# Optimization experiments

Measured on AMD Instinct MI355X. Metric: run time of the kernel, lower is better.

## Reference

```python
import jax, jax.numpy as jnp
import numpy as np

NDIM = (256, 256, 256)
NMIN = (-1.0, -1.0, -1.0)
NMAX = (1.0, 1.0, 1.0)
NDELTA = tuple((NMAX[i] - NMIN[i]) / (NDIM[i] - 1.0) for i in range(3))
MIN_DEG, MAX_DEG = 0, 10
ANNEALED_ALPHA = 1.0
EPS = 1e-12


def compute_grad(grid):
    # central differences on the voxel grid with edge padding -> [N, 3]
    g = grid.reshape(NDIM[0], NDIM[1], NDIM[2])
    p = jnp.pad(g, ((1, 1), (1, 1), (1, 1)), mode='edge')
    dx = (p[2:, 1:-1, 1:-1] - p[:-2, 1:-1, 1:-1]) / (2.0 * NDELTA[0])
    dy = (p[1:-1, 2:, 1:-1] - p[1:-1, :-2, 1:-1]) / (2.0 * NDELTA[1])
    dz = (p[1:-1, 1:-1, 2:] - p[1:-1, 1:-1, :-2]) / (2.0 * NDELTA[2])
    return jnp.stack([dx, dy, dz], axis=-1).reshape(-1, 3)


def trilinear3(data, pts):
    # data: [N, 4] flattened voxel features, pts: [B, 3] -> [B, 4]
    x = (pts[..., 0] - NMIN[0]) / NDELTA[0]
    y = (pts[..., 1] - NMIN[1]) / NDELTA[1]
    z = (pts[..., 2] - NMIN[2]) / NDELTA[2]
    x0f = jnp.floor(x); y0f = jnp.floor(y); z0f = jnp.floor(z)
    xd = (x - x0f)[..., None]
    yd = (y - y0f)[..., None]
    zd = (z - z0f)[..., None]
    x0 = jnp.clip(x0f.astype(jnp.int32), 0, NDIM[0] - 1)
    x1 = jnp.clip(x0f.astype(jnp.int32) + 1, 0, NDIM[0] - 1)
    y0 = jnp.clip(y0f.astype(jnp.int32), 0, NDIM[1] - 1)
    y1 = jnp.clip(y0f.astype(jnp.int32) + 1, 0, NDIM[1] - 1)
    z0 = jnp.clip(z0f.astype(jnp.int32), 0, NDIM[2] - 1)
    z1 = jnp.clip(z0f.astype(jnp.int32) + 1, 0, NDIM[2] - 1)
    sYZ, sZ = NDIM[1] * NDIM[2], NDIM[2]
    gat = lambda i, j, k: data[sYZ * i + sZ * j + k]
    c00 = gat(x0, y0, z0) * (1 - xd) + gat(x1, y0, z0) * xd
    c01 = gat(x0, y0, z1) * (1 - xd) + gat(x1, y0, z1) * xd
    c10 = gat(x0, y1, z0) * (1 - xd) + gat(x1, y1, z0) * xd
    c11 = gat(x0, y1, z1) * (1 - xd) + gat(x1, y1, z1) * xd
    c0 = c00 * (1 - yd) + c10 * yd
    c1 = c01 * (1 - yd) + c11 * yd
    return c0 * (1 - zd) + c1 * zd


def annealed_pos_enc(x, alpha):
    # nerfies-style windowed positional encoding with identity concat
    bands = jnp.arange(MIN_DEG, MAX_DEG, dtype=x.dtype)  # [D]
    scales = 2.0 ** bands
    xb = x[..., None, :] * scales[:, None]               # [..., D, 3]
    four = jnp.sin(jnp.stack([xb, xb + 0.5 * jnp.pi], axis=-2))  # [..., D, 2, 3]
    w = jnp.clip(alpha - bands, 0.0, 1.0)
    w = 0.5 * (1.0 - jnp.cos(jnp.pi * w))                # cosine easing window
    four = four * w[:, None, None]
    four = four.reshape(x.shape[:-1] + (-1,))            # [..., D*6]
    return jnp.concatenate([x, four], axis=-1)           # [..., 3 + D*6]


def mlp(feats, w0, b0, w1, b1, w2, b2, w3, b3, wo, bo):
    # net_depth=4, skip_layer=2 -> concat inputs after layer index 2
    h = jax.nn.relu(feats @ w0 + b0)
    h = jax.nn.relu(h @ w1 + b1)
    h = jax.nn.relu(h @ w2 + b2)
    h = jnp.concatenate([h, feats], axis=-1)
    h = jax.nn.relu(h @ w3 + b3)
    return h @ wo + bo


def safe_l2_norm(v):
    return jnp.sqrt(jnp.sum(v * v, axis=-1, keepdims=True) + EPS)


def setup_inputs() -> dict:
    key = jax.random.key(0)
    ks = jax.random.split(key, 8)
    B = 1048576
    N = NDIM[0] * NDIM[1] * NDIM[2]
    x = jax.random.uniform(ks[0], (B, 3), jnp.float32, -1.0, 1.0)
    grid = jax.random.normal(ks[1], (N, 1), jnp.float32)
    glorot = lambda k, fi, fo: jax.random.normal(k, (fi, fo), jnp.float32) * jnp.sqrt(2.0 / (fi + fo))
    return {
        'x': x, 'grid': grid,
        'w0': glorot(ks[2], 63, 128), 'b0': jnp.zeros((128,), jnp.float32),
        'w1': glorot(ks[3], 128, 128), 'b1': jnp.zeros((128,), jnp.float32),
        'w2': glorot(ks[4], 128, 128), 'b2': jnp.zeros((128,), jnp.float32),
        'w3': glorot(ks[5], 191, 128), 'b3': jnp.zeros((128,), jnp.float32),
        'wo': jax.random.normal(ks[6], (128, 3), jnp.float32) * 1e-5,  # output_init normal(1e-5)
        'bo': jnp.zeros((3,), jnp.float32),
    }


def reference(x, grid, w0, b0, w1, b1, w2, b2, w3, b3, wo, bo):
    data = jnp.concatenate([grid, compute_grad(grid)], axis=-1)  # [N, 4]
    ret = trilinear3(data, x)                                    # [B, 4]
    feats = annealed_pos_enc(x[:, None], ANNEALED_ALPHA * MAX_DEG)  # [B, 1, 63]
    raw = mlp(feats, w0, b0, w1, b1, w2, b2, w3, b3, wo, bo)[:, 0]  # [B, 3]
    # residual + direct output: rotate gradient vector by axis-angle raw
    theta = safe_l2_norm(raw)
    e = raw / theta
    cond = ret[..., 1:]
    a = safe_l2_norm(cond)
    v = cond / a
    rot = a * (jnp.cos(theta) * v + jnp.sin(theta) * jnp.cross(e, v)
               + (1.0 - jnp.cos(theta)) * jnp.sum(e * v, axis=-1, keepdims=True) * e)
    return (ret[..., :1], ret[..., 1:], rot)
```

## Files before the change

### kernel.cpp

```cpp
#include <hip/hip_runtime.h>


typedef __attribute__((ext_vector_type(4))) float f4;
typedef long long llg;

__device__ __forceinline__ float bf2f(unsigned int u) {
    union { float f; unsigned int i; } v; v.i = u << 16; return v.f;
}
__device__ __forceinline__ unsigned short f2bf(float f) {
    union { float f; unsigned int i; } v; v.f = f;
    unsigned int x = v.i;
    return (unsigned short)((x + 0x7fffu + ((x >> 16) & 1u)) >> 16);
}
__device__ __forceinline__ unsigned int pkbf(float a, float b) {
    unsigned int r;
    asm("v_cvt_pk_bf16_f32 %0, %1, %2" : "=v"(r) : "v"(a), "v"(b));
    return r;
}
__device__ __forceinline__ float gv(const float* __restrict__ g, int i, int j, int k) {
    return g[(i * 256 + j) * 256 + k];
}
__device__ __forceinline__ int featmap(int kp) {
    if (kp < 3) return kp;
    if (kp == 3) return -1;
    const int m = kp - 4, b = m / 6, r = m - 6 * b, d = r >> 1, c = r & 1;
    return 3 + 6 * b + 3 * c + d;
}

#define WS_TOTAL 67584
#define SWZ_BLOCKS 264
#define DG_BLOCKS 8192
#define DG_OFF_SH 131072
#define WS_NEED (262144ull + 16777216ull * 8ull)
#define WO_SCALE 8192.0f
#define WO_INV   (1.0f / 8192.0f)

__global__ __launch_bounds__(256) void prep(
    const float* __restrict__ g,
    const float* __restrict__ w0, const float* __restrict__ w1,
    const float* __restrict__ w2, const float* __restrict__ w3,
    const float* __restrict__ wo,
    unsigned char* __restrict__ ws8, unsigned short* __restrict__ dg,
    int do_dgrid)
{
    const int bid = blockIdx.x;
    if (bid < SWZ_BLOCKS) {
        int idx = bid * 256 + threadIdx.x;
        const float* src; int base, NT, Kact, Nact, ld;
        if (idx < 8192)       { src = w0; base = 0;     NT = 8; Kact = 64;  Nact = 128; ld = 128; }
        else if (idx < 24576) { src = w1; base = 8192;  NT = 8; Kact = 128; Nact = 128; ld = 128; }
        else if (idx < 40960) { src = w2; base = 24576; NT = 8; Kact = 128; Nact = 128; ld = 128; }
        else if (idx < 65536) { src = w3; base = 40960; NT = 8; Kact = 192; Nact = 128; ld = 128; }
        else                  { src = wo; base = 65536; NT = 1; Kact = 128; Nact = 3;   ld = 3;   }
        int local = idx - base;
        int j = local & 7;
        int lane = (local >> 3) & 63;
        int chunk = local >> 9;
        int nt = chunk % NT, kt = chunk / NT;
        int k = kt * 32 + ((lane >> 4) << 3) + j;
        int n = nt * 16 + (lane & 15);
        float v = 0.0f;
        if (k < Kact && n < Nact) {
            int ko = k;
            if (base == 0)            ko = featmap(k);
            else if (base == 40960 && k >= 128) {
                int f = featmap(k - 128);
                ko = (f < 0) ? -1 : 128 + f;
            }
            if (ko >= 0) v = src[ko * ld + n];
            if (base == 65536) v *= WO_SCALE;
        }
        int p = __builtin_amdgcn_cvt_pk_fp8_f32(v, v, 0, false);
        ws8[idx] = (unsigned char)(p & 0xff);
    } else if (do_dgrid) {
        const int t  = (bid - SWZ_BLOCKS) * 256 + threadIdx.x;
        const int k0 = (t & 31) << 3;
        const int j  = (t >> 5) & 255;
        const int i  = t >> 13;
        const float* row = g + (i * 256 + j) * 256;
        const float* rxp = g + (min(i + 1, 255) * 256 + j) * 256;
        const float* rxm = g + (max(i - 1, 0)   * 256 + j) * 256;
        const float* ryp = g + (i * 256 + min(j + 1, 255)) * 256;
        const float* rym = g + (i * 256 + max(j - 1, 0))   * 256;
        float se[8], sxp[8], sxm[8], syp[8], sym[8];
        {
            f4 a = *(const f4*)(row + k0), b = *(const f4*)(row + k0 + 4);
            #pragma unroll
            for (int q = 0; q < 4; ++q) { se[q] = a[q]; se[q + 4] = b[q]; }
            a = *(const f4*)(rxp + k0); b = *(const f4*)(rxp + k0 + 4);
            #pragma unroll
            for (int q = 0; q < 4; ++q) { sxp[q] = a[q]; sxp[q + 4] = b[q]; }
            a = *(const f4*)(rxm + k0); b = *(const f4*)(rxm + k0 + 4);
            #pragma unroll
            for (int q = 0; q < 4; ++q) { sxm[q] = a[q]; sxm[q + 4] = b[q]; }
            a = *(const f4*)(ryp + k0); b = *(const f4*)(ryp + k0 + 4);
            #pragma unroll
            for (int q = 0; q < 4; ++q) { syp[q] = a[q]; syp[q + 4] = b[q]; }
            a = *(const f4*)(rym + k0); b = *(const f4*)(rym + k0 + 4);
            #pragma unroll
            for (int q = 0; q < 4; ++q) { sym[q] = a[q]; sym[q + 4] = b[q]; }
        }
        float zv[10];
        zv[0] = row[max(k0 - 1, 0)];
        #pragma unroll
        for (int q = 0; q < 8; ++q) zv[q + 1] = se[q];
        zv[9] = row[min(k0 + 8, 255)];
        unsigned int o[16];
        #pragma unroll
        for (int q = 0; q < 8; ++q) {
            o[q * 2 + 0] = pkbf(se[q], (sxp[q] - sxm[q]) * 63.75f);
            o[q * 2 + 1] = pkbf((syp[q] - sym[q]) * 63.75f, (zv[q + 2] - zv[q]) * 63.75f);
        }
        unsigned short* dst = dg + (size_t)(((i * 256 + j) * 256 + k0)) * 4;
        #pragma unroll
        for (int q = 0; q < 4; ++q)
            *(uint4*)(dst + q * 8) = *(const uint4*)(&o[q * 4]);
    }
}

#define HSTRIDE_B 136
#define FSTRIDE_B 88
#define WV_BYTES (32 * HSTRIDE_B + 32 * FSTRIDE_B)

template<bool FAST>
__global__ __launch_bounds__(256, 5) void voxmlp(
    const float* __restrict__ x, const float* __restrict__ grid,
    const unsigned char* __restrict__ ws8, const unsigned short* __restrict__ dg,
    const float* __restrict__ b0, const float* __restrict__ b1,
    const float* __restrict__ b2, const float* __restrict__ b3,
    const float* __restrict__ bo,
    float* __restrict__ out, int B)
{
    __shared__ unsigned char smem[WV_BYTES * 4];

    const int lane = threadIdx.x & 63;
    const int wave = threadIdx.x >> 6;
    const int quad = lane >> 4;
    const int lm   = lane & 15;
    unsigned char* bufH = smem + wave * WV_BYTES;
    unsigned char* fbuf = bufH + 32 * HSTRIDE_B;

    const int pbase = blockIdx.x * 128 + wave * 32;

    const int p2   = lane & 31;
    const int role = lane >> 5;
    const int pid  = pbase + p2;

    const float px = x[pid * 3 + 0];
    const float py = x[pid * 3 + 1];
    const float pz = x[pid * 3 + 2];

    if (role == 0) {
        const float fx = (px + 1.0f) * 127.5f;
        const float fy = (py + 1.0f) * 127.5f;
        const float fz = (pz + 1.0f) * 127.5f;
        const float fx0 = floorf(fx), fy0 = floorf(fy), fz0 = floorf(fz);
        const float xd = fx - fx0, yd = fy - fy0, zd = fz - fz0;
        const int ix0 = min(max((int)fx0, 0), 255);
        const int iy0 = min(max((int)fy0, 0), 255);
        const int iz0 = min(max((int)fz0, 0), 255);
        const int ix1 = min(ix0 + 1, 255);
        const int iy1 = min(iy0 + 1, 255);
        const int iz1 = min(iz0 + 1, 255);

        float ret0 = 0.f, c1 = 0.f, c2 = 0.f, c3 = 0.f;
        if (FAST) {
            #pragma unroll
            for (int c = 0; c < 8; ++c) {
                const int i = (c & 4) ? ix1 : ix0;
                const int j = (c & 2) ? iy1 : iy0;
                const int k = (c & 1) ? iz1 : iz0;
                const float wgt = ((c & 4) ? xd : 1.0f - xd) *
                                  ((c & 2) ? yd : 1.0f - yd) *
                                  ((c & 1) ? zd : 1.0f - zd);
                const uint2 w = *(const uint2*)(dg + (size_t)((i * 256 + j) * 256 + k) * 4);
                ret0 = fmaf(wgt, bf2f(w.x & 0xffffu), ret0);
                c1   = fmaf(wgt, bf2f(w.x >> 16),     c1);
                c2   = fmaf(wgt, bf2f(w.y & 0xffffu), c2);
                c3   = fmaf(wgt, bf2f(w.y >> 16),     c3);
            }
        } else {
            #pragma unroll
            for (int c = 0; c < 8; ++c) {
                const int i = (c & 4) ? ix1 : ix0;
                const int j = (c & 2) ? iy1 : iy0;
                const int k = (c & 1) ? iz1 : iz0;
                const float wgt = ((c & 4) ? xd : 1.0f - xd) *
                                  ((c & 2) ? yd : 1.0f - yd) *
                                  ((c & 1) ? zd : 1.0f - zd);
                const float v  = gv(grid, i, j, k);
                const float gx = (gv(grid, min(i + 1, 255), j, k) - gv(grid, max(i - 1, 0), j, k)) * 63.75f;
                const float gy = (gv(grid, i, min(j + 1, 255), k) - gv(grid, i, max(j - 1, 0), k)) * 63.75f;
                const float gz = (gv(grid, i, j, min(k + 1, 255)) - gv(grid, i, j, max(k - 1, 0))) * 63.75f;
                ret0 = fmaf(wgt, v,  ret0);
                c1   = fmaf(wgt, gx, c1);
                c2   = fmaf(wgt, gy, c2);
                c3   = fmaf(wgt, gz, c3);
            }
        }
        out[pid] = ret0;
        out[B + pid * 3 + 0] = c1;
        out[B + pid * 3 + 1] = c2;
        out[B + pid * 3 + 2] = c3;
        float* cst = (float*)(fbuf + p2 * FSTRIDE_B + 64);
        cst[0] = c1; cst[1] = c2; cst[2] = c3;
    } else {
        float s[64];
        s[0] = px; s[1] = py; s[2] = pz; s[3] = 0.0f;
        const float crd[3] = {px, py, pz};
        float sc = 1.0f;
        #pragma unroll
        for (int b = 0; b < 10; ++b) {
            #pragma unroll
            for (int d = 0; d < 3; ++d) {
                float sv, cv;
                __sincosf(crd[d] * sc, &sv, &cv);
                s[4 + b * 6 + d * 2 + 0] = sv;
                s[4 + b * 6 + d * 2 + 1] = cv;
            }
            sc *= 2.0f;
        }
        unsigned int dw[16];
        #pragma unroll
        for (int i = 0; i < 16; ++i) {
            int d = __builtin_amdgcn_cvt_pk_fp8_f32(s[4 * i + 0], s[4 * i + 1], 0, false);
            d     = __builtin_amdgcn_cvt_pk_fp8_f32(s[4 * i + 2], s[4 * i + 3], d, true);
            dw[i] = (unsigned int)d;
        }
        unsigned char* fb = fbuf + p2 * FSTRIDE_B;
        #pragma unroll
        for (int i = 0; i < 4; ++i) {
            uint2 pk; pk.x = dw[2 * i]; pk.y = dw[2 * i + 1];
            *(uint2*)(fb + i * 8) = pk;
        }
        #pragma unroll
        for (int i = 4; i < 8; ++i) {
            uint2 pk; pk.x = dw[2 * i]; pk.y = dw[2 * i + 1];
            *(uint2*)(fb + i * 8) = pk;
        }
    }
    __builtin_amdgcn_s_barrier();

    llg af[2][6];
    const int arow0 = lm * HSTRIDE_B + quad * 8;
    const int frow0 = lm * FSTRIDE_B + quad * 8;

    auto store_tile = [&](f4 acc, int pt, int ut) {
        int d = __builtin_amdgcn_cvt_pk_fp8_f32(fmaxf(acc[0], 0.f), fmaxf(acc[1], 0.f), 0, false);
        d     = __builtin_amdgcn_cvt_pk_fp8_f32(fmaxf(acc[2], 0.f), fmaxf(acc[3], 0.f), d, true);
        *(int*)(bufH + (pt * 16 + lm) * HSTRIDE_B + ut * 16 + quad * 4) = d;
    };

    #pragma unroll
    for (int pt = 0; pt < 2; ++pt)
        #pragma unroll
        for (int kt = 0; kt < 2; ++kt)
            af[pt][kt] = *(const llg*)(fbuf + pt * 16 * FSTRIDE_B + frow0 + kt * 32);
    #pragma unroll
    for (int ut = 0; ut < 8; ++ut) {
        llg wf[2];
        #pragma unroll
        for (int kt = 0; kt < 2; ++kt)
            wf[kt] = *(const llg*)(ws8 + 0 + (((kt * 8 + ut) * 64 + lane) << 3));
        const f4 bias = *(const f4*)(b0 + ut * 16 + quad * 4);
        #pragma unroll
        for (int pt = 0; pt < 2; ++pt) {
            f4 acc = bias;
            #pragma unroll
            for (int kt = 0; kt < 2; ++kt)
                acc = __builtin_amdgcn_mfma_f32_16x16x32_fp8_fp8(wf[kt], af[pt][kt], acc, 0, 0, 0);
            store_tile(acc, pt, ut);
        }
    }
    __builtin_amdgcn_s_barrier();

    #pragma unroll
    for (int layer = 0; layer < 2; ++layer) {
        const unsigned char* wsl = ws8 + (layer == 0 ? 8192 : 24576);
        const float* bias_p = (layer == 0) ? b1 : b2;
        #pragma unroll
        for (int pt = 0; pt < 2; ++pt)
            #pragma unroll
            for (int kt = 0; kt < 4; ++kt)
                af[pt][kt] = *(const llg*)(bufH + pt * 16 * HSTRIDE_B + arow0 + kt * 32);
        #pragma unroll
        for (int ut = 0; ut < 8; ++ut) {
            llg wf[4];
            #pragma unroll
            for (int kt = 0; kt < 4; ++kt)
                wf[kt] = *(const llg*)(wsl + (((kt * 8 + ut) * 64 + lane) << 3));
            const f4 bias = *(const f4*)(bias_p + ut * 16 + quad * 4);
            #pragma unroll
            for (int pt = 0; pt < 2; ++pt) {
                f4 acc = bias;
                #pragma unroll
                for (int kt = 0; kt < 4; ++kt)
                    acc = __builtin_amdgcn_mfma_f32_16x16x32_fp8_fp8(wf[kt], af[pt][kt], acc, 0, 0, 0);
                store_tile(acc, pt, ut);
            }
        }
        __builtin_amdgcn_s_barrier();
    }

    #pragma unroll
    for (int pt = 0; pt < 2; ++pt) {
        #pragma unroll
        for (int kt = 0; kt < 4; ++kt)
            af[pt][kt] = *(const llg*)(bufH + pt * 16 * HSTRIDE_B + arow0 + kt * 32);
        #pragma unroll
        for (int kk = 0; kk < 2; ++kk)
            af[pt][4 + kk] = *(const llg*)(fbuf + pt * 16 * FSTRIDE_B + frow0 + kk * 32);
    }
    #pragma unroll
    for (int ut = 0; ut < 8; ++ut) {
        llg wf[6];
        #pragma unroll
        for (int kt = 0; kt < 6; ++kt)
            wf[kt] = *(const llg*)(ws8 + 40960 + (((kt * 8 + ut) * 64 + lane) << 3));
        const f4 bias = *(const f4*)(b3 + ut * 16 + quad * 4);
        #pragma unroll
        for (int pt = 0; pt < 2; ++pt) {
            f4 acc = bias;
            #pragma unroll
            for (int kt = 0; kt < 6; ++kt)
                acc = __builtin_amdgcn_mfma_f32_16x16x32_fp8_fp8(wf[kt], af[pt][kt], acc, 0, 0, 0);
            store_tile(acc, pt, ut);
        }
    }
    __builtin_amdgcn_s_barrier();

    #pragma unroll
    for (int pt = 0; pt < 2; ++pt)
        #pragma unroll
        for (int kt = 0; kt < 4; ++kt)
            af[pt][kt] = *(const llg*)(bufH + pt * 16 * HSTRIDE_B + arow0 + kt * 32);
    llg wf[4];
    #pragma unroll
    for (int kt = 0; kt < 4; ++kt)
        wf[kt] = *(const llg*)(ws8 + 65536 + ((kt * 64 + lane) << 3));

    const float bo0 = bo[0], bo1 = bo[1], bo2 = bo[2];
    #pragma unroll
    for (int pt = 0; pt < 2; ++pt) {
        f4 acc = {0.f, 0.f, 0.f, 0.f};
        #pragma unroll
        for (int kt = 0; kt < 4; ++kt)
            acc = __builtin_amdgcn_mfma_f32_16x16x32_fp8_fp8(wf[kt], af[pt][kt], acc, 0, 0, 0);

        const int pp = pt * 16 + lm;
        const float* cst = (const float*)(fbuf + pp * FSTRIDE_B + 64);
        const float g1 = cst[0], g2 = cst[1], g3 = cst[2];
        const float r0 = acc[0] * WO_INV + bo0;
        const float r1 = acc[1] * WO_INV + bo1;
        const float r2 = acc[2] * WO_INV + bo2;
        const float theta = sqrtf(fmaf(r0, r0, fmaf(r1, r1, r2 * r2)) + 1e-12f);
        const float it = __builtin_amdgcn_rcpf(theta);
        const float e0 = r0 * it, e1 = r1 * it, e2 = r2 * it;
        const float a = sqrtf(fmaf(g1, g1, fmaf(g2, g2, g3 * g3)) + 1e-12f);
        const float ia = __builtin_amdgcn_rcpf(a);
        const float v0 = g1 * ia, v1 = g2 * ia, v2 = g3 * ia;
        float st, ct;
        __sincosf(theta, &st, &ct);
        const float cx = e1 * v2 - e2 * v1;
        const float cy = e2 * v0 - e0 * v2;
        const float cz = e0 * v1 - e1 * v0;
        const float om = (1.0f - ct) * (e0 * v0 + e1 * v1 + e2 * v2);
        if (quad == 0) {
            const int pid2 = pbase + pp;
            out[4 * B + pid2 * 3 + 0] = a * (ct * v0 + st * cx + om * e0);
            out[4 * B + pid2 * 3 + 1] = a * (ct * v1 + st * cy + om * e1);
            out[4 * B + pid2 * 3 + 2] = a * (ct * v2 + st * cz + om * e2);
        }
    }
}

extern "C" void kernel_launch(void* const* d_in, const int* in_sizes, int n_in,
                              void* d_out, int out_size, void* d_ws, size_t ws_size,
                              hipStream_t stream)
{
    const float* x    = (const float*)d_in[0];
    const float* grid = (const float*)d_in[1];
    const float* w0   = (const float*)d_in[2];
    const float* b0   = (const float*)d_in[3];
    const float* w1   = (const float*)d_in[4];
    const float* b1   = (const float*)d_in[5];
    const float* w2   = (const float*)d_in[6];
    const float* b2   = (const float*)d_in[7];
    const float* w3   = (const float*)d_in[8];
    const float* b3   = (const float*)d_in[9];
    const float* wo   = (const float*)d_in[10];
    const float* bo   = (const float*)d_in[11];
    float* out = (float*)d_out;
    unsigned char* ws8 = (unsigned char*)d_ws;
    unsigned short* dg = (unsigned short*)d_ws + DG_OFF_SH;

    const int B = in_sizes[0] / 3;
    const int fast = (ws_size >= WS_NEED) ? 1 : 0;
    const int nprep = fast ? (SWZ_BLOCKS + DG_BLOCKS) : SWZ_BLOCKS;
    prep<<<nprep, 256, 0, stream>>>(grid, w0, w1, w2, w3, wo, ws8, dg, fast);
    if (fast)
        voxmlp<true><<<B / 128, 256, 0, stream>>>(x, grid, ws8, dg, b0, b1, b2, b3, bo, out, B);
    else
        voxmlp<false><<<B / 128, 256, 0, stream>>>(x, grid, ws8, dg, b0, b1, b2, b3, bo, out, B);
}
```

Measured before the change: 368.1 us.

## Keep MLP hidden activations in registers via permuted weight K-order

The hidden-layer activations now stay in VGPRs between MFMA layers instead of being written to and re-read from LDS. To allow this, the prep kernel permutes the K dimension of the hidden weight matrices (hidperm) so each lane's MFMA output already matches the B-operand layout of the next layer. This removes the LDS round-trips and the per-layer barriers. It also shrinks shared memory, raises the occupancy hint from 5 to 6, and reorders dgrid block indices, at the cost of more register pressure.

```diff
diff --git a/kernel.cpp b/kernel.cpp
--- a/kernel.cpp
+++ b/kernel.cpp
@@ -6,11 +6,6 @@
 
 __device__ __forceinline__ float bf2f(unsigned int u) {
     union { float f; unsigned int i; } v; v.i = u << 16; return v.f;
-}
-__device__ __forceinline__ unsigned short f2bf(float f) {
-    union { float f; unsigned int i; } v; v.f = f;
-    unsigned int x = v.i;
-    return (unsigned short)((x + 0x7fffu + ((x >> 16) & 1u)) >> 16);
 }
 __device__ __forceinline__ unsigned int pkbf(float a, float b) {
     unsigned int r;
@@ -25,6 +20,18 @@
     if (kp == 3) return -1;
     const int m = kp - 4, b = m / 6, r = m - 6 * b, d = r >> 1, c = r & 1;
     return 3 + 6 * b + 3 * c + d;
+}
+__device__ __forceinline__ int hidperm(int k) {
+    const int kt = k >> 5, q = (k >> 3) & 3, j = k & 7;
+    return 32 * kt + ((j >> 2) << 4) + (q << 2) + (j & 3);
+}
+__device__ __forceinline__ llg mkllg(unsigned int lo, unsigned int hi) {
+    return (llg)(((unsigned long long)lo) | (((unsigned long long)hi) << 32));
+}
+__device__ __forceinline__ unsigned int pack8(f4 acc) {
+    int d = __builtin_amdgcn_cvt_pk_fp8_f32(fmaxf(acc[0], 0.f), fmaxf(acc[1], 0.f), 0, false);
+    d     = __builtin_amdgcn_cvt_pk_fp8_f32(fmaxf(acc[2], 0.f), fmaxf(acc[3], 0.f), d, true);
+    return (unsigned int)d;
 }
 
 #define WS_TOTAL 67584
@@ -61,11 +68,18 @@
         int n = nt * 16 + (lane & 15);
         float v = 0.0f;
         if (k < Kact && n < Nact) {
-            int ko = k;
-            if (base == 0)            ko = featmap(k);
-            else if (base == 40960 && k >= 128) {
-                int f = featmap(k - 128);
-                ko = (f < 0) ? -1 : 128 + f;
+            int ko;
+            if (base == 0) {
+                ko = featmap(k);
+            } else if (base == 40960) {
+                if (k >= 128) {
+                    int f = featmap(k - 128);
+                    ko = (f < 0) ? -1 : 128 + f;
+                } else {
+                    ko = hidperm(k);
+                }
+            } else {
+                ko = hidperm(k);
             }
             if (ko >= 0) v = src[ko * ld + n];
             if (base == 65536) v *= WO_SCALE;
@@ -73,7 +87,9 @@
         int p = __builtin_amdgcn_cvt_pk_fp8_f32(v, v, 0, false);
         ws8[idx] = (unsigned char)(p & 0xff);
     } else if (do_dgrid) {
-        const int t  = (bid - SWZ_BLOCKS) * 256 + threadIdx.x;
+        int rb = bid - SWZ_BLOCKS;
+        rb = (rb & 7) * 1024 + (rb >> 3);
+        const int t  = rb * 256 + threadIdx.x;
         const int k0 = (t & 31) << 3;
         const int j  = (t >> 5) & 255;
         const int i  = t >> 13;
@@ -118,12 +134,11 @@
     }
 }
 
-#define HSTRIDE_B 136
 #define FSTRIDE_B 88
-#define WV_BYTES (32 * HSTRIDE_B + 32 * FSTRIDE_B)
+#define WV_BYTES (32 * FSTRIDE_B)
 
 template<bool FAST>
-__global__ __launch_bounds__(256, 5) void voxmlp(
+__global__ __launch_bounds__(256, 6) void voxmlp(
     const float* __restrict__ x, const float* __restrict__ grid,
     const unsigned char* __restrict__ ws8, const unsigned short* __restrict__ dg,
     const float* __restrict__ b0, const float* __restrict__ b1,
@@ -137,8 +152,7 @@
     const int wave = threadIdx.x >> 6;
     const int quad = lane >> 4;
     const int lm   = lane & 15;
-    unsigned char* bufH = smem + wave * WV_BYTES;
-    unsigned char* fbuf = bufH + 32 * HSTRIDE_B;
+    unsigned char* fbuf = smem + wave * WV_BYTES;
 
     const int pbase = blockIdx.x * 128 + wave * 32;
 
@@ -229,60 +243,45 @@
         }
         unsigned char* fb = fbuf + p2 * FSTRIDE_B;
         #pragma unroll
-        for (int i = 0; i < 4; ++i) {
+        for (int i = 0; i < 8; ++i) {
             uint2 pk; pk.x = dw[2 * i]; pk.y = dw[2 * i + 1];
             *(uint2*)(fb + i * 8) = pk;
         }
-        #pragma unroll
-        for (int i = 4; i < 8; ++i) {
-            uint2 pk; pk.x = dw[2 * i]; pk.y = dw[2 * i + 1];
-            *(uint2*)(fb + i * 8) = pk;
-        }
     }
     __builtin_amdgcn_s_barrier();
 
-    llg af[2][6];
-    const int arow0 = lm * HSTRIDE_B + quad * 8;
     const int frow0 = lm * FSTRIDE_B + quad * 8;
 
-    auto store_tile = [&](f4 acc, int pt, int ut) {
-        int d = __builtin_amdgcn_cvt_pk_fp8_f32(fmaxf(acc[0], 0.f), fmaxf(acc[1], 0.f), 0, false);
-        d     = __builtin_amdgcn_cvt_pk_fp8_f32(fmaxf(acc[2], 0.f), fmaxf(acc[3], 0.f), d, true);
-        *(int*)(bufH + (pt * 16 + lm) * HSTRIDE_B + ut * 16 + quad * 4) = d;
-    };
-
-    #pragma unroll
-    for (int pt = 0; pt < 2; ++pt)
-        #pragma unroll
-        for (int kt = 0; kt < 2; ++kt)
-            af[pt][kt] = *(const llg*)(fbuf + pt * 16 * FSTRIDE_B + frow0 + kt * 32);
-    #pragma unroll
-    for (int ut = 0; ut < 8; ++ut) {
-        llg wf[2];
-        #pragma unroll
-        for (int kt = 0; kt < 2; ++kt)
-            wf[kt] = *(const llg*)(ws8 + 0 + (((kt * 8 + ut) * 64 + lane) << 3));
-        const f4 bias = *(const f4*)(b0 + ut * 16 + quad * 4);
-        #pragma unroll
-        for (int pt = 0; pt < 2; ++pt) {
-            f4 acc = bias;
+    unsigned int actA[2][8];
+    unsigned int actB[2][8];
+
+    {
+        llg ff[2][2];
+        #pragma unroll
+        for (int pt = 0; pt < 2; ++pt)
             #pragma unroll
             for (int kt = 0; kt < 2; ++kt)
-                acc = __builtin_amdgcn_mfma_f32_16x16x32_fp8_fp8(wf[kt], af[pt][kt], acc, 0, 0, 0);
-            store_tile(acc, pt, ut);
+                ff[pt][kt] = *(const llg*)(fbuf + pt * 16 * FSTRIDE_B + frow0 + kt * 32);
+        #pragma unroll
+        for (int ut = 0; ut < 8; ++ut) {
+            llg wf[2];
+            #pragma unroll
+            for (int kt = 0; kt < 2; ++kt)
+                wf[kt] = *(const llg*)(ws8 + 0 + (((kt * 8 + ut) * 64 + lane) << 3));
+            const f4 bias = *(const f4*)(b0 + ut * 16 + quad * 4);
+            #pragma unroll
+            for (int pt = 0; pt < 2; ++pt) {
+                f4 acc = bias;
+                #pragma unroll
+                for (int kt = 0; kt < 2; ++kt)
+                    acc = __builtin_amdgcn_mfma_f32_16x16x32_fp8_fp8(wf[kt], ff[pt][kt], acc, 0, 0, 0);
+                actA[pt][ut] = pack8(acc);
+            }
         }
     }
-    __builtin_amdgcn_s_barrier();
-
-    #pragma unroll
-    for (int layer = 0; layer < 2; ++layer) {
-        const unsigned char* wsl = ws8 + (layer == 0 ? 8192 : 24576);
-        const float* bias_p = (layer == 0) ? b1 : b2;
-        #pragma unroll
-        for (int pt = 0; pt < 2; ++pt)
-            #pragma unroll
-            for (int kt = 0; kt < 4; ++kt)
-                af[pt][kt] = *(const llg*)(bufH + pt * 16 * HSTRIDE_B + arow0 + kt * 32);
+
+    auto hidden = [&](const unsigned char* wsl, const float* bias_p,
+                      const unsigned int (&src)[2][8], unsigned int (&dst)[2][8]) {
         #pragma unroll
         for (int ut = 0; ut < 8; ++ut) {
             llg wf[4];
@@ -295,45 +294,44 @@
                 f4 acc = bias;
                 #pragma unroll
                 for (int kt = 0; kt < 4; ++kt)
-                    acc = __builtin_amdgcn_mfma_f32_16x16x32_fp8_fp8(wf[kt], af[pt][kt], acc, 0, 0, 0);
-                store_tile(acc, pt, ut);
-            }
-        }
-        __builtin_amdgcn_s_barrier();
+                    acc = __builtin_amdgcn_mfma_f32_16x16x32_fp8_fp8(
+                            wf[kt], mkllg(src[pt][2 * kt], src[pt][2 * kt + 1]), acc, 0, 0, 0);
+                dst[pt][ut] = pack8(acc);
+            }
+        }
+    };
+    hidden(ws8 + 8192,  b1, actA, actB);
+    hidden(ws8 + 24576, b2, actB, actA);
+
+    {
+        llg ff[2][2];
+        #pragma unroll
+        for (int pt = 0; pt < 2; ++pt)
+            #pragma unroll
+            for (int kk = 0; kk < 2; ++kk)
+                ff[pt][kk] = *(const llg*)(fbuf + pt * 16 * FSTRIDE_B + frow0 + kk * 32);
+        #pragma unroll
+        for (int ut = 0; ut < 8; ++ut) {
+            llg wf[6];
+            #pragma unroll
+            for (int kt = 0; kt < 6; ++kt)
+                wf[kt] = *(const llg*)(ws8 + 40960 + (((kt * 8 + ut) * 64 + lane) << 3));
+            const f4 bias = *(const f4*)(b3 + ut * 16 + quad * 4);
+            #pragma unroll
+            for (int pt = 0; pt < 2; ++pt) {
+                f4 acc = bias;
+                #pragma unroll
+                for (int kt = 0; kt < 4; ++kt)
+                    acc = __builtin_amdgcn_mfma_f32_16x16x32_fp8_fp8(
+                            wf[kt], mkllg(actA[pt][2 * kt], actA[pt][2 * kt + 1]), acc, 0, 0, 0);
+                #pragma unroll
+                for (int kk = 0; kk < 2; ++kk)
+                    acc = __builtin_amdgcn_mfma_f32_16x16x32_fp8_fp8(wf[4 + kk], ff[pt][kk], acc, 0, 0, 0);
+                actB[pt][ut] = pack8(acc);
+            }
+        }
     }
 
-    #pragma unroll
-    for (int pt = 0; pt < 2; ++pt) {
-        #pragma unroll
-        for (int kt = 0; kt < 4; ++kt)
-            af[pt][kt] = *(const llg*)(bufH + pt * 16 * HSTRIDE_B + arow0 + kt * 32);
-        #pragma unroll
-        for (int kk = 0; kk < 2; ++kk)
-            af[pt][4 + kk] = *(const llg*)(fbuf + pt * 16 * FSTRIDE_B + frow0 + kk * 32);
-    }
-    #pragma unroll
-    for (int ut = 0; ut < 8; ++ut) {
-        llg wf[6];
-        #pragma unroll
-        for (int kt = 0; kt < 6; ++kt)
-            wf[kt] = *(const llg*)(ws8 + 40960 + (((kt * 8 + ut) * 64 + lane) << 3));
-        const f4 bias = *(const f4*)(b3 + ut * 16 + quad * 4);
-        #pragma unroll
-        for (int pt = 0; pt < 2; ++pt) {
-            f4 acc = bias;
-            #pragma unroll
-            for (int kt = 0; kt < 6; ++kt)
-                acc = __builtin_amdgcn_mfma_f32_16x16x32_fp8_fp8(wf[kt], af[pt][kt], acc, 0, 0, 0);
-            store_tile(acc, pt, ut);
-        }
-    }
-    __builtin_amdgcn_s_barrier();
-
-    #pragma unroll
-    for (int pt = 0; pt < 2; ++pt)
-        #pragma unroll
-        for (int kt = 0; kt < 4; ++kt)
-            af[pt][kt] = *(const llg*)(bufH + pt * 16 * HSTRIDE_B + arow0 + kt * 32);
     llg wf[4];
     #pragma unroll
     for (int kt = 0; kt < 4; ++kt)
@@ -345,7 +343,8 @@
         f4 acc = {0.f, 0.f, 0.f, 0.f};
         #pragma unroll
         for (int kt = 0; kt < 4; ++kt)
-            acc = __builtin_amdgcn_mfma_f32_16x16x32_fp8_fp8(wf[kt], af[pt][kt], acc, 0, 0, 0);
+            acc = __builtin_amdgcn_mfma_f32_16x16x32_fp8_fp8(
+                    wf[kt], mkllg(actB[pt][2 * kt], actB[pt][2 * kt + 1]), acc, 0, 0, 0);
 
         const int pp = pt * 16 + lm;
         const float* cst = (const float*)(fbuf + pp * FSTRIDE_B + 64);
```

Result: slower. 422.2 us (+14.7%).
